# Optimization experiments

Measured on AMD Instinct MI355X. Metric: run time of the kernel, lower is better.

Reference implementation:

```python
import jax, jax.numpy as jnp
import numpy as np

N, E, ESM, H_DIM, HEADS, LAYERS = 20000, 640000, 1280, 256, 8, 3
C = H_DIM // HEADS  # per-head channels = 32
B, M = 4096, 8


def setup_inputs() -> dict:
    key = jax.random.key(0)
    ks = jax.random.split(key, 24)
    s = lambda i, *shp: jax.random.normal(ks[i], shp, dtype=jnp.float32) * 0.02
    inp = {
        'x': jax.random.normal(ks[0], (N, ESM), dtype=jnp.float32),
        'edge_index': jax.random.randint(ks[1], (2, E), 0, N),
        'sites': jax.random.randint(ks[2], (B, M), 0, N),
        'mut_onehot': jax.random.normal(ks[3], (B, M, 20), dtype=jnp.float32),
        'mask': jnp.ones((B, M), dtype=bool),
        # params
        'in_W': s(4, ESM, H_DIM), 'in_b': jnp.zeros((H_DIM,), jnp.float32),
        'gat_W': s(5, LAYERS, H_DIM, HEADS * C),
        'att_src': s(6, LAYERS, HEADS, C), 'att_dst': s(7, LAYERS, HEADS, C),
        'gat_b': jnp.zeros((LAYERS, H_DIM), jnp.float32),
        'ln_g': jnp.ones((LAYERS, H_DIM), jnp.float32),
        'ln_b': jnp.zeros((LAYERS, H_DIM), jnp.float32),
        'me_W1': s(8, 20, H_DIM), 'me_b1': jnp.zeros((H_DIM,), jnp.float32),
        'me_W2': s(9, H_DIM, H_DIM), 'me_b2': jnp.zeros((H_DIM,), jnp.float32),
        'pool_q': jax.random.normal(ks[10], (H_DIM,), dtype=jnp.float32),
        'key_W': s(11, H_DIM, H_DIM), 'key_b': jnp.zeros((H_DIM,), jnp.float32),
        'mlp_W1': s(12, H_DIM, H_DIM // 2), 'mlp_b1': jnp.zeros((H_DIM // 2,), jnp.float32),
        'mlp_W2': s(13, H_DIM // 2, 1), 'mlp_b2': jnp.zeros((1,), jnp.float32),
    }
    return inp


def layer_norm(h, g, b, eps=1e-5):
    mu = h.mean(-1, keepdims=True)
    var = ((h - mu) ** 2).mean(-1, keepdims=True)
    return (h - mu) * jax.lax.rsqrt(var + eps) * g + b


def gat_conv(h, src, dst, W, a_src, a_dst, b):
    # PyG GATConv: linear -> per-node attn logits -> edge leaky_relu -> segment softmax over dst -> scatter-sum
    xh = (h @ W).reshape(N, HEADS, C)
    al_s = (xh * a_src).sum(-1)  # [N,H]
    al_d = (xh * a_dst).sum(-1)
    alpha = jax.nn.leaky_relu(al_s[src] + al_d[dst], negative_slope=0.2)  # [E',H]
    mx = jax.ops.segment_max(alpha, dst, num_segments=N)
    ea = jnp.exp(alpha - mx[dst])
    denom = jax.ops.segment_sum(ea, dst, num_segments=N)
    w = ea / (denom[dst] + 1e-16)
    msg = xh[src] * w[:, :, None]  # [E',H,C]
    out = jax.ops.segment_sum(msg, dst, num_segments=N)
    return out.reshape(N, HEADS * C) + b


def reference(x, edge_index, sites, mut_onehot, mask, in_W, in_b, gat_W, att_src, att_dst,
              gat_b, ln_g, ln_b, me_W1, me_b1, me_W2, me_b2, pool_q, key_W, key_b,
              mlp_W1, mlp_b1, mlp_W2, mlp_b2):
    # GATConv default add_self_loops=True
    loops = jnp.arange(N, dtype=edge_index.dtype)
    src = jnp.concatenate([edge_index[0], loops])
    dst = jnp.concatenate([edge_index[1], loops])
    # encode_graph (eval mode: dropout = identity)
    h = x @ in_W + in_b
    for i in range(LAYERS):
        h_new = gat_conv(h, src, dst, gat_W[i], att_src[i][None], att_dst[i][None], gat_b[i])
        h_new = jax.nn.elu(h_new)
        h = layer_norm(h_new + h, ln_g[i], ln_b[i])
    # predict_batch
    site_embeds = h[sites]  # [B,M,H_DIM]
    mut_embeds = jax.nn.relu(mut_onehot @ me_W1 + me_b1) @ me_W2 + me_b2
    combined = site_embeds + mut_embeds
    keys = combined @ key_W + key_b
    scores = (pool_q * keys).sum(-1) / np.sqrt(H_DIM).astype(np.float32)
    scores = jnp.where(mask, scores, -jnp.inf)
    weights = jax.nn.softmax(scores, axis=-1)[..., None]
    pooled = (weights * combined).sum(axis=1)  # [B,H_DIM]
    out = jax.nn.relu(pooled @ mlp_W1 + mlp_b1) @ mlp_W2 + mlp_b2
    return out.squeeze(-1)
```

## Files before the change

### kernel.cpp

```cpp
#include <hip/hip_runtime.h>
#include <math.h>

#define N_NODES 20000
#define N_EDGES 640000
#define E_TOT   (N_EDGES + N_NODES)
#define HD 256
#define NH 8
#define CH 32
#define NB 4096
#define NM 8

typedef short bf16x8 __attribute__((ext_vector_type(8)));
typedef float f32x4  __attribute__((ext_vector_type(4)));

__device__ __forceinline__ ushort f2bf(float f) {
  uint u = __float_as_uint(f);
  u += 0x7FFFu + ((u >> 16) & 1u);
  return (ushort)(u >> 16);
}
__device__ __forceinline__ float bf2f(ushort s) {
  return __uint_as_float(((uint)s) << 16);
}

__global__ __launch_bounds__(256) void k_wtrans(
    const float* __restrict__ W, ushort* __restrict__ WT,
    int K, int N, int strideW, int strideWT)
{
  __shared__ float tile[64][65];
  const float* Wp = W + (size_t)blockIdx.z * strideW;
  ushort* WTp = WT + (size_t)blockIdx.z * strideWT;
  int n0 = blockIdx.x * 64, k0 = blockIdx.y * 64;
  int t = threadIdx.x;
  int c = t & 63, r0 = (t >> 6) * 16;
#pragma unroll
  for (int i = 0; i < 16; ++i)
    tile[r0 + i][c] = Wp[(size_t)(k0 + r0 + i) * N + n0 + c];
  __syncthreads();
#pragma unroll
  for (int i = 0; i < 16; ++i)
    WTp[(size_t)(n0 + r0 + i) * K + k0 + c] = f2bf(tile[c][r0 + i]);
}

template<int MODE>
__global__ __launch_bounds__(256, 2) void k_gemm_mfma(
    const void* __restrict__ Ain, const ushort* __restrict__ BT,
    const float* __restrict__ bias, float* __restrict__ Cf,
    ushort* __restrict__ Cb, int M, int K)
{
  __shared__ ushort As[128 * 32];
  __shared__ ushort Bs[128 * 32];
  const int t = threadIdx.x;
  const int n0 = blockIdx.x * 128;
  const int m0 = blockIdx.y * 128;
  const int wave = t >> 6, lane = t & 63;
  const int wm = (wave & 1) * 64, wn = (wave >> 1) * 64;
  const int lm = lane & 15, quad = lane >> 4;

  f32x4 acc[4][4];
#pragma unroll
  for (int mi = 0; mi < 4; ++mi)
#pragma unroll
    for (int ni = 0; ni < 4; ++ni) acc[mi][ni] = (f32x4){0.f, 0.f, 0.f, 0.f};

  int rowc[2], jc[2], arc[2];
#pragma unroll
  for (int cch = 0; cch < 2; ++cch) {
    int id = t + cch * 256;
    rowc[cch] = id >> 2;
    jc[cch]   = id & 3;
    arc[cch]  = min(m0 + rowc[cch], M - 1);
  }

  float4 pa0[2], pa1[2];
  uint4  paB[2];
  uint4  pb[2];

#define LOAD_TILE(K0)                                                          \
  {                                                                            \
    _Pragma("unroll")                                                          \
    for (int cch = 0; cch < 2; ++cch) {                                        \
      if (MODE == 0) {                                                         \
        const float* src = (const float*)Ain + (size_t)arc[cch] * K + (K0) + jc[cch] * 8; \
        pa0[cch] = *(const float4*)src;                                        \
        pa1[cch] = *(const float4*)(src + 4);                                  \
      } else {                                                                 \
        const ushort* src = (const ushort*)Ain + (size_t)arc[cch] * K + (K0) + jc[cch] * 8; \
        paB[cch] = *(const uint4*)src;                                         \
      }                                                                        \
      pb[cch] = *(const uint4*)(BT + (size_t)(n0 + rowc[cch]) * K + (K0) + jc[cch] * 8); \
    }                                                                          \
  }

  LOAD_TILE(0);

  for (int k0 = 0; k0 < K; k0 += 32) {
#pragma unroll
    for (int cch = 0; cch < 2; ++cch) {
      int row = rowc[cch];
      int sw = (jc[cch] ^ (row & 3)) * 8;
      if (MODE == 0) {
        uint4 p;
        p.x = (uint)f2bf(pa0[cch].x) | ((uint)f2bf(pa0[cch].y) << 16);
        p.y = (uint)f2bf(pa0[cch].z) | ((uint)f2bf(pa0[cch].w) << 16);
        p.z = (uint)f2bf(pa1[cch].x) | ((uint)f2bf(pa1[cch].y) << 16);
        p.w = (uint)f2bf(pa1[cch].z) | ((uint)f2bf(pa1[cch].w) << 16);
        *(uint4*)&As[row * 32 + sw] = p;
      } else {
        *(uint4*)&As[row * 32 + sw] = paB[cch];
      }
      *(uint4*)&Bs[row * 32 + sw] = pb[cch];
    }
    __syncthreads();
    if (k0 + 32 < K) LOAD_TILE(k0 + 32);

    bf16x8 af[4], bfr[4];
#pragma unroll
    for (int mi = 0; mi < 4; ++mi) {
      int row = wm + mi * 16 + lm;
      af[mi] = *(const bf16x8*)&As[row * 32 + ((quad ^ (row & 3)) << 3)];
    }
#pragma unroll
    for (int ni = 0; ni < 4; ++ni) {
      int row = wn + ni * 16 + lm;
      bfr[ni] = *(const bf16x8*)&Bs[row * 32 + ((quad ^ (row & 3)) << 3)];
    }
#pragma unroll
    for (int mi = 0; mi < 4; ++mi)
#pragma unroll
      for (int ni = 0; ni < 4; ++ni)
        acc[mi][ni] = __builtin_amdgcn_mfma_f32_16x16x32_bf16(af[mi], bfr[ni], acc[mi][ni], 0, 0, 0);
    __syncthreads();
  }
#undef LOAD_TILE

#pragma unroll
  for (int mi = 0; mi < 4; ++mi) {
#pragma unroll
    for (int r = 0; r < 4; ++r) {
      int row = m0 + wm + mi * 16 + quad * 4 + r;
      if (row < M) {
#pragma unroll
        for (int ni = 0; ni < 4; ++ni) {
          int col = n0 + wn + ni * 16 + lm;
          float vv = acc[mi][ni][r];
          if (MODE == 0) {
            float o = vv + bias[col];
            Cf[(size_t)row * HD + col] = o;
            Cb[(size_t)row * HD + col] = f2bf(o);
          } else {
            Cb[(size_t)row * HD + col] = f2bf(vv);
          }
        }
      }
    }
  }
}

__global__ void k_setconst(int* __restrict__ p, int n, int v) {
  int i = blockIdx.x * blockDim.x + threadIdx.x;
  if (i < n) p[i] = v;
}

__global__ void k_count(const int* __restrict__ dst, int* __restrict__ cnt) {
  int e = blockIdx.x * blockDim.x + threadIdx.x;
  if (e < N_EDGES) atomicAdd(&cnt[dst[e]], 1);
}

__global__ __launch_bounds__(1024) void k_scanA(const int* __restrict__ cnt,
                                                int* __restrict__ sc, int* __restrict__ tot) {
  __shared__ int wsum[16];
  int g = blockIdx.x * 1024 + threadIdx.x;
  int lane = threadIdx.x & 63, w = threadIdx.x >> 6;
  int v = (g < N_NODES) ? cnt[g] : 0;
#pragma unroll
  for (int off = 1; off < 64; off <<= 1) {
    int u = __shfl_up(v, off);
    if (lane >= off) v += u;
  }
  if (lane == 63) wsum[w] = v;
  __syncthreads();
  if (w == 0) {
    int s = (lane < 16) ? wsum[lane] : 0;
#pragma unroll
    for (int off = 1; off < 16; off <<= 1) {
      int u = __shfl_up(s, off);
      if (lane >= off) s += u;
    }
    if (lane < 16) wsum[lane] = s;
  }
  __syncthreads();
  if (w > 0) v += wsum[w - 1];
  if (g < N_NODES) sc[g] = v;
  if (threadIdx.x == 1023) tot[blockIdx.x] = v;
}

__global__ void k_scanB(int* __restrict__ tot) {
  int lane = threadIdx.x;
  int v = (lane < 20) ? tot[lane] : 0;
#pragma unroll
  for (int off = 1; off < 32; off <<= 1) {
    int u = __shfl_up(v, off);
    if (lane >= off) v += u;
  }
  int e = __shfl_up(v, 1);
  if (lane == 0) e = 0;
  if (lane < 20) tot[lane] = e;
}

__global__ __launch_bounds__(1024) void k_scanC(const int* __restrict__ sc,
                                                const int* __restrict__ tot,
                                                int* __restrict__ row_ptr) {
  int g = blockIdx.x * 1024 + threadIdx.x;
  if (g < N_NODES) row_ptr[g + 1] = sc[g] + tot[blockIdx.x];
  if (g == 0) row_ptr[0] = 0;
}

__global__ void k_fill(const int* __restrict__ ei, const int* __restrict__ row_ptr,
                       int* __restrict__ fill, int* __restrict__ csr) {
  int idx = blockIdx.x * blockDim.x + threadIdx.x;
  if (idx >= E_TOT) return;
  int s, d;
  if (idx < N_EDGES) { s = ei[idx]; d = ei[N_EDGES + idx]; }
  else               { s = idx - N_EDGES; d = s; }
  int p = atomicAdd(&fill[d], 1);
  csr[row_ptr[d] + p] = s;
}

__global__ void k_attn(const ushort* __restrict__ xh,
                       const float* __restrict__ att_s,
                       const float* __restrict__ att_d,
                       float* __restrict__ al_s, float* __restrict__ al_d)
{
  int idx = blockIdx.x * blockDim.x + threadIdx.x;
  if (idx >= N_NODES * NH) return;
  int hh = idx & 7;
  const ushort* row = xh + (size_t)(idx >> 3) * HD + hh * CH;
  const float4* a4  = (const float4*)(att_s + hh * CH);
  const float4* b4  = (const float4*)(att_d + hh * CH);
  float s = 0.f, d = 0.f;
#pragma unroll
  for (int q = 0; q < 8; ++q) {
    ushort4 xv = *(const ushort4*)(row + q * 4);
    float4 a = a4[q], b = b4[q];
    float v0 = bf2f(xv.x), v1 = bf2f(xv.y), v2 = bf2f(xv.z), v3 = bf2f(xv.w);
    s += v0 * a.x + v1 * a.y + v2 * a.z + v3 * a.w;
    d += v0 * b.x + v1 * b.y + v2 * b.z + v3 * b.w;
  }
  al_s[idx] = s;
  al_d[idx] = d;
}

__global__ __launch_bounds__(256) void k_aggregate(
    const ushort* __restrict__ xh, const float* __restrict__ al_s,
    const float* __restrict__ al_d, const int* __restrict__ row_ptr,
    const int* __restrict__ csr_src, const float* __restrict__ gat_b,
    const float* __restrict__ ln_g, const float* __restrict__ ln_b,
    float* __restrict__ h, ushort* __restrict__ h_bf)
{
  __shared__ float s_ea[4][64][9];
  __shared__ int   s_src[4][64];
  __shared__ int   s_deg[4];
  const int t = threadIdx.x;
  const int w = t >> 6, lane = t & 63;
  const int node = blockIdx.x * 4 + w;
  const int base = row_ptr[node];
  const int deg  = row_ptr[node + 1] - base;
  if (lane == 0) s_deg[w] = deg;
  __syncthreads();
  const int maxdeg = max(max(s_deg[0], s_deg[1]), max(s_deg[2], s_deg[3]));
  const int chunks = (maxdeg + 63) >> 6;

  float ald[8];
  {
    float4 a0 = *(const float4*)(al_d + (size_t)node * NH);
    float4 a1 = *(const float4*)(al_d + (size_t)node * NH + 4);
    ald[0] = a0.x; ald[1] = a0.y; ald[2] = a0.z; ald[3] = a0.w;
    ald[4] = a1.x; ald[5] = a1.y; ald[6] = a1.z; ald[7] = a1.w;
  }
  const int hh = lane >> 3;
  float4 acc = {0.f, 0.f, 0.f, 0.f};
  float den = 0.f;

  for (int c = 0; c < chunks; ++c) {
    const int cs = c << 6;
    int n = deg - cs; n = (n > 64) ? 64 : n;
    if (lane < n) {
      int s = csr_src[base + cs + lane];
      s_src[w][lane] = s;
      float4 b0 = *(const float4*)(al_s + (size_t)s * NH);
      float4 b1 = *(const float4*)(al_s + (size_t)s * NH + 4);
      float al[8] = {b0.x, b0.y, b0.z, b0.w, b1.x, b1.y, b1.z, b1.w};
#pragma unroll
      for (int q = 0; q < 8; ++q) {
        float a = al[q] + ald[q];
        a = fmaxf(a, 0.2f * a);
        s_ea[w][lane][q] = __expf(a);
      }
    }
    __syncthreads();
    for (int e = 0; e < n; ++e) {
      float wa = s_ea[w][e][hh];
      int s = s_src[w][e];
      den += wa;
      ushort4 xv = *(const ushort4*)(xh + (size_t)s * HD + lane * 4);
      acc.x = fmaf(wa, bf2f(xv.x), acc.x);
      acc.y = fmaf(wa, bf2f(xv.y), acc.y);
      acc.z = fmaf(wa, bf2f(xv.z), acc.z);
      acc.w = fmaf(wa, bf2f(xv.w), acc.w);
    }
    __syncthreads();
  }

  const float inv = 1.f / (den + 1e-16f);
  float4 g4 = *(const float4*)(gat_b + lane * 4);
  float4 v;
  v.x = acc.x * inv + g4.x;
  v.y = acc.y * inv + g4.y;
  v.z = acc.z * inv + g4.z;
  v.w = acc.w * inv + g4.w;
  v.x = (v.x > 0.f) ? v.x : (__expf(v.x) - 1.f);
  v.y = (v.y > 0.f) ? v.y : (__expf(v.y) - 1.f);
  v.z = (v.z > 0.f) ? v.z : (__expf(v.z) - 1.f);
  v.w = (v.w > 0.f) ? v.w : (__expf(v.w) - 1.f);
  float4 hres = *(const float4*)(h + (size_t)node * HD + lane * 4);
  v.x += hres.x; v.y += hres.y; v.z += hres.z; v.w += hres.w;

  float sum = v.x + v.y + v.z + v.w;
#pragma unroll
  for (int off = 32; off > 0; off >>= 1) sum += __shfl_xor(sum, off);
  const float mu = sum * (1.f / 256.f);
  float dx = v.x - mu, dy = v.y - mu, dz = v.z - mu, dw = v.w - mu;
  float ss = dx * dx + dy * dy + dz * dz + dw * dw;
#pragma unroll
  for (int off = 32; off > 0; off >>= 1) ss += __shfl_xor(ss, off);
  const float r = rsqrtf(ss * (1.f / 256.f) + 1e-5f);
  float4 lg = *(const float4*)(ln_g + lane * 4);
  float4 lb = *(const float4*)(ln_b + lane * 4);
  float4 o;
  o.x = dx * r * lg.x + lb.x;
  o.y = dy * r * lg.y + lb.y;
  o.z = dz * r * lg.z + lb.z;
  o.w = dw * r * lg.w + lb.w;
  *(float4*)(h + (size_t)node * HD + lane * 4) = o;
  ushort4 ob;
  ob.x = f2bf(o.x); ob.y = f2bf(o.y); ob.z = f2bf(o.z); ob.w = f2bf(o.w);
  *(ushort4*)(h_bf + (size_t)node * HD + lane * 4) = ob;
}

__global__ __launch_bounds__(256) void k_qk(const float* __restrict__ key_W,
                                            const float* __restrict__ key_b,
                                            const float* __restrict__ pool_q,
                                            float* __restrict__ qk)
{
  __shared__ float sq[HD];
  int t = threadIdx.x;
  sq[t] = pool_q[t];
  __syncthreads();
  float a = 0.f;
  for (int j = 0; j < HD; ++j) a = fmaf(key_W[(size_t)t * HD + j], sq[j], a);
  qk[t] = a;
  if (t == 0) {
    float qb = 0.f;
    for (int j = 0; j < HD; ++j) qb += sq[j] * key_b[j];
    qk[HD] = qb;
  }
}

__global__ __launch_bounds__(256) void k_mut1(
    const float* __restrict__ onehot, const float* __restrict__ W1,
    const float* __restrict__ b1, ushort* __restrict__ m1)
{
  __shared__ float s_oh[128][20];
  const int t = threadIdx.x;
  const int r0 = blockIdx.x * 128;
  float wreg[20];
#pragma unroll
  for (int j = 0; j < 20; ++j) wreg[j] = W1[j * HD + t];
  const float bb = b1[t];
  for (int i = t; i < 128 * 20; i += 256)
    s_oh[i / 20][i % 20] = onehot[(size_t)r0 * 20 + i];
  __syncthreads();
  for (int r = 0; r < 128; ++r) {
    float v = bb;
#pragma unroll
    for (int j = 0; j < 20; ++j) v = fmaf(s_oh[r][j], wreg[j], v);
    m1[(size_t)(r0 + r) * HD + t] = f2bf(fmaxf(v, 0.f));
  }
}

__global__ __launch_bounds__(256, 2) void k_gemm_mut2(
    const ushort* __restrict__ m1, const ushort* __restrict__ W2T,
    const float* __restrict__ me_b2, const float* __restrict__ h,
    const int* __restrict__ sites, const unsigned char* __restrict__ mask8,
    const float* __restrict__ qk, float* __restrict__ pooled)
{
  __shared__ ushort As[64 * 32];
  __shared__ ushort Bs[256 * 32];
  __shared__ float s_part[64][4];
  __shared__ float s_w[64];
  __shared__ int   s_site[64];
  const int t = threadIdx.x;
  const int rows0 = blockIdx.x * 64;
  const int wave = t >> 6, lane = t & 63;
  const int wn = wave * 64;
  const int lm = lane & 15, quad = lane >> 4;

  if (t < 64) s_site[t] = sites[rows0 + t];

  f32x4 acc[4][4];
#pragma unroll
  for (int mi = 0; mi < 4; ++mi)
#pragma unroll
    for (int ni = 0; ni < 4; ++ni) acc[mi][ni] = (f32x4){0.f, 0.f, 0.f, 0.f};

  const int a_row = t >> 2, a_j = t & 3;
  uint4 pa;
  uint4 pbv[4];
#define LOAD_MUT(K0)                                                           \
  {                                                                            \
    pa = *(const uint4*)(m1 + (size_t)(rows0 + a_row) * HD + (K0) + a_j * 8);  \
    _Pragma("unroll")                                                          \
    for (int p = 0; p < 4; ++p) {                                              \
      int id = t + p * 256;                                                    \
      int row = id >> 2, j = id & 3;                                           \
      pbv[p] = *(const uint4*)(W2T + (size_t)row * HD + (K0) + j * 8);         \
    }                                                                          \
  }

  LOAD_MUT(0);
  for (int k0 = 0; k0 < HD; k0 += 32) {
    {
      int sw = (a_j ^ (a_row & 3)) * 8;
      *(uint4*)&As[a_row * 32 + sw] = pa;
#pragma unroll
      for (int p = 0; p < 4; ++p) {
        int id = t + p * 256;
        int row = id >> 2, j = id & 3;
        *(uint4*)&Bs[row * 32 + ((j ^ (row & 3)) * 8)] = pbv[p];
      }
    }
    __syncthreads();
    if (k0 + 32 < HD) LOAD_MUT(k0 + 32);

    bf16x8 af[4], bfr[4];
#pragma unroll
    for (int mi = 0; mi < 4; ++mi) {
      int row = mi * 16 + lm;
      af[mi] = *(const bf16x8*)&As[row * 32 + ((quad ^ (row & 3)) << 3)];
    }
#pragma unroll
    for (int ni = 0; ni < 4; ++ni) {
      int row = wn + ni * 16 + lm;
      bfr[ni] = *(const bf16x8*)&Bs[row * 32 + ((quad ^ (row & 3)) << 3)];
    }
#pragma unroll
    for (int mi = 0; mi < 4; ++mi)
#pragma unroll
      for (int ni = 0; ni < 4; ++ni)
        acc[mi][ni] = __builtin_amdgcn_mfma_f32_16x16x32_bf16(af[mi], bfr[ni], acc[mi][ni], 0, 0, 0);
    __syncthreads();
  }
#undef LOAD_MUT

  float pscore[4][4];
#pragma unroll
  for (int mi = 0; mi < 4; ++mi)
#pragma unroll
    for (int r = 0; r < 4; ++r) pscore[mi][r] = 0.f;

#pragma unroll
  for (int ni = 0; ni < 4; ++ni) {
    int col = wn + ni * 16 + lm;
    float qkc = qk[col];
    float b2c = me_b2[col];
#pragma unroll
    for (int mi = 0; mi < 4; ++mi) {
#pragma unroll
      for (int r = 0; r < 4; ++r) {
        int row = mi * 16 + quad * 4 + r;
        float c = acc[mi][ni][r] + b2c + h[(size_t)s_site[row] * HD + col];
        acc[mi][ni][r] = c;
        pscore[mi][r] = fmaf(c, qkc, pscore[mi][r]);
      }
    }
  }
#pragma unroll
  for (int mi = 0; mi < 4; ++mi)
#pragma unroll
    for (int r = 0; r < 4; ++r) {
      float p = pscore[mi][r];
      p += __shfl_xor(p, 8); p += __shfl_xor(p, 4);
      p += __shfl_xor(p, 2); p += __shfl_xor(p, 1);
      pscore[mi][r] = p;
    }
  if (lm == 0) {
#pragma unroll
    for (int mi = 0; mi < 4; ++mi)
#pragma unroll
      for (int r = 0; r < 4; ++r)
        s_part[mi * 16 + quad * 4 + r][wave] = pscore[mi][r];
  }
  __syncthreads();
  if (t < 64) {
    float s = s_part[t][0] + s_part[t][1] + s_part[t][2] + s_part[t][3];
    s = (s + qk[HD]) * 0.0625f;
    int grow = rows0 + t;
    bool mb;
    if (mask8[1] != 0) mb = mask8[grow] != 0;
    else               mb = ((const int*)mask8)[grow] != 0;
    s_w[t] = mb ? s : -INFINITY;
  }
  __syncthreads();
  if (t < 8) {
    float e[NM], mx = -INFINITY, den = 0.f;
#pragma unroll
    for (int m = 0; m < NM; ++m) mx = fmaxf(mx, s_w[t * NM + m]);
#pragma unroll
    for (int m = 0; m < NM; ++m) { e[m] = __expf(s_w[t * NM + m] - mx); den += e[m]; }
    float inv = 1.f / den;
#pragma unroll
    for (int m = 0; m < NM; ++m) s_w[t * NM + m] = e[m] * inv;
  }
  __syncthreads();
#pragma unroll
  for (int ni = 0; ni < 4; ++ni) {
    int col = wn + ni * 16 + lm;
#pragma unroll
    for (int mi = 0; mi < 4; ++mi) {
      float pp = 0.f;
#pragma unroll
      for (int r = 0; r < 4; ++r)
        pp = fmaf(s_w[mi * 16 + quad * 4 + r], acc[mi][ni][r], pp);
      pp += __shfl_xor(pp, 16);
      int b = mi * 2 + (quad >> 1);
      if ((quad & 1) == 0)
        pooled[(size_t)(blockIdx.x * 8 + b) * HD + col] = pp;
    }
  }
}

__global__ __launch_bounds__(128) void k_mlp(
    const float* __restrict__ pooled, const float* __restrict__ W1,
    const float* __restrict__ b1, const float* __restrict__ W2,
    const float* __restrict__ b2, float* __restrict__ out)
{
  __shared__ float s_p[16][256];
  __shared__ float s_red[16][128];
  const int t = threadIdx.x;
  const int r0 = blockIdx.x * 16;
  for (int i = t; i < 16 * 256; i += 128) {
    int r = i >> 8, cc = i & 255;
    s_p[r][cc] = pooled[(size_t)(r0 + r) * HD + cc];
  }
  __syncthreads();
  float accm[16];
#pragma unroll
  for (int r = 0; r < 16; ++r) accm[r] = 0.f;
  for (int i = 0; i < 256; ++i) {
    float w = W1[(size_t)i * 128 + t];
#pragma unroll
    for (int r = 0; r < 16; ++r) accm[r] = fmaf(s_p[r][i], w, accm[r]);
  }
  float w2 = W2[t], bb1 = b1[t];
#pragma unroll
  for (int r = 0; r < 16; ++r) s_red[r][t] = fmaxf(accm[r] + bb1, 0.f) * w2;
  __syncthreads();
  if (t < 16) {
    float s = b2[0];
    for (int j = 0; j < 128; ++j) s += s_red[t][j];
    out[r0 + t] = s;
  }
}

extern "C" void kernel_launch(void* const* d_in, const int* in_sizes, int n_in,
                              void* d_out, int out_size, void* d_ws, size_t ws_size,
                              hipStream_t stream) {
  (void)in_sizes; (void)n_in; (void)out_size; (void)ws_size;
  const float* x        = (const float*)d_in[0];
  const int*   ei       = (const int*)d_in[1];
  const int*   sites    = (const int*)d_in[2];
  const float* onehot   = (const float*)d_in[3];
  const unsigned char* mask = (const unsigned char*)d_in[4];
  const float* in_W     = (const float*)d_in[5];
  const float* in_b     = (const float*)d_in[6];
  const float* gat_W    = (const float*)d_in[7];
  const float* att_src  = (const float*)d_in[8];
  const float* att_dst  = (const float*)d_in[9];
  const float* gat_b    = (const float*)d_in[10];
  const float* ln_g     = (const float*)d_in[11];
  const float* ln_b     = (const float*)d_in[12];
  const float* me_W1    = (const float*)d_in[13];
  const float* me_b1    = (const float*)d_in[14];
  const float* me_W2    = (const float*)d_in[15];
  const float* me_b2    = (const float*)d_in[16];
  const float* pool_q   = (const float*)d_in[17];
  const float* key_W    = (const float*)d_in[18];
  const float* key_b    = (const float*)d_in[19];
  const float* mlp_W1   = (const float*)d_in[20];
  const float* mlp_b1   = (const float*)d_in[21];
  const float* mlp_W2   = (const float*)d_in[22];
  const float* mlp_b2   = (const float*)d_in[23];
  float* outp = (float*)d_out;

  char* w = (char*)d_ws;
  float*  h       = (float*)(w + 0);
  ushort* h_bf    = (ushort*)(w + 20480000);
  ushort* xh_bf   = (ushort*)(w + 30720000);
  float*  al_s    = (float*)(w + 40960000);
  float*  al_d    = (float*)(w + 41600000);
  int*    row_ptr = (int*)  (w + 42240000);
  int*    cnt     = (int*)  (w + 42320128);
  int*    csr     = (int*)  (w + 42400128);
  float*  qk      = (float*)(w + 45040128);
  float*  pooled  = (float*)(w + 45041408);
  int*    sc      = (int*)pooled;
  int*    tot     = sc + N_NODES;
  ushort* in_WT   = (ushort*)((char*)pooled + 131072);
  ushort* gat_WT  = (ushort*)((char*)pooled + 786432);
  ushort* m1      = (ushort*)(w + 20480000);
  ushort* me_W2T  = (ushort*)(w + 40960000);

  k_wtrans<<<dim3(4, 20, 1), 256, 0, stream>>>(in_W, in_WT, 1280, HD, 0, 0);
  k_wtrans<<<dim3(4, 4, 3), 256, 0, stream>>>(gat_W, gat_WT, HD, HD, HD * HD, HD * HD);

  k_gemm_mfma<0><<<dim3(2, 157), 256, 0, stream>>>(x, in_WT, in_b, h, h_bf, N_NODES, 1280);

  k_setconst<<<(N_NODES + 255) / 256, 256, 0, stream>>>(cnt, N_NODES, 1);
  k_count<<<(N_EDGES + 255) / 256, 256, 0, stream>>>(ei + N_EDGES, cnt);
  k_scanA<<<20, 1024, 0, stream>>>(cnt, sc, tot);
  k_scanB<<<1, 64, 0, stream>>>(tot);
  k_scanC<<<20, 1024, 0, stream>>>(sc, tot, row_ptr);
  k_setconst<<<(N_NODES + 255) / 256, 256, 0, stream>>>(cnt, N_NODES, 0);
  k_fill<<<(E_TOT + 255) / 256, 256, 0, stream>>>(ei, row_ptr, cnt, csr);

  for (int l = 0; l < 3; ++l) {
    k_gemm_mfma<1><<<dim3(2, 157), 256, 0, stream>>>(h_bf, gat_WT + (size_t)l * HD * HD,
                                                     nullptr, nullptr, xh_bf, N_NODES, HD);
    k_attn<<<(N_NODES * NH + 255) / 256, 256, 0, stream>>>(xh_bf, att_src + l * NH * CH,
                                                           att_dst + l * NH * CH, al_s, al_d);
    k_aggregate<<<N_NODES / 4, 256, 0, stream>>>(xh_bf, al_s, al_d, row_ptr, csr,
                                                 gat_b + l * HD, ln_g + l * HD, ln_b + l * HD,
                                                 h, h_bf);
  }

  k_wtrans<<<dim3(4, 4, 1), 256, 0, stream>>>(me_W2, me_W2T, HD, HD, 0, 0);
  k_mut1<<<NB * NM / 128, 256, 0, stream>>>(onehot, me_W1, me_b1, m1);
  k_qk<<<1, 256, 0, stream>>>(key_W, key_b, pool_q, qk);
  k_gemm_mut2<<<NB * NM / 64, 256, 0, stream>>>(m1, me_W2T, me_b2, h, sites, mask, qk, pooled);
  k_mlp<<<NB / 16, 128, 0, stream>>>(pooled, mlp_W1, mlp_b1, mlp_W2, mlp_b2, outp);
}
```

Before: 699.7 us.

## Shrink GEMM M-tile to 64, drop register prefetch, split aggregate edges across half-waves

The node GEMM's M-tile drops from 128 to 64 rows, with launch bounds raised to 4 blocks per CU and the grid doubled, for more occupancy and better load balance. The register prefetch of the next K tile is removed from both GEMMs, simplifying them at the cost of less overlap between loads and MFMA. The aggregation kernel now has each half-wave handle alternate edges with 16-byte loads of 8 channels, combining the halves with a shuffle. This doubles memory-level parallelism per gather but adds a reduction and leaves half the lanes idle during the stores.

```diff
diff --git a/kernel.cpp b/kernel.cpp
--- a/kernel.cpp
+++ b/kernel.cpp
@@ -42,80 +42,56 @@
 }
 
 template<int MODE>
-__global__ __launch_bounds__(256, 2) void k_gemm_mfma(
+__global__ __launch_bounds__(256, 4) void k_gemm_mfma(
     const void* __restrict__ Ain, const ushort* __restrict__ BT,
     const float* __restrict__ bias, float* __restrict__ Cf,
     ushort* __restrict__ Cb, int M, int K)
 {
-  __shared__ ushort As[128 * 32];
+  __shared__ ushort As[64 * 32];
   __shared__ ushort Bs[128 * 32];
   const int t = threadIdx.x;
   const int n0 = blockIdx.x * 128;
-  const int m0 = blockIdx.y * 128;
+  const int m0 = blockIdx.y * 64;
   const int wave = t >> 6, lane = t & 63;
-  const int wm = (wave & 1) * 64, wn = (wave >> 1) * 64;
+  const int wm = (wave & 1) * 32, wn = (wave >> 1) * 64;
   const int lm = lane & 15, quad = lane >> 4;
 
-  f32x4 acc[4][4];
-#pragma unroll
-  for (int mi = 0; mi < 4; ++mi)
+  f32x4 acc[2][4];
+#pragma unroll
+  for (int mi = 0; mi < 2; ++mi)
 #pragma unroll
     for (int ni = 0; ni < 4; ++ni) acc[mi][ni] = (f32x4){0.f, 0.f, 0.f, 0.f};
 
-  int rowc[2], jc[2], arc[2];
-#pragma unroll
-  for (int cch = 0; cch < 2; ++cch) {
-    int id = t + cch * 256;
-    rowc[cch] = id >> 2;
-    jc[cch]   = id & 3;
-    arc[cch]  = min(m0 + rowc[cch], M - 1);
-  }
-
-  float4 pa0[2], pa1[2];
-  uint4  paB[2];
-  uint4  pb[2];
-
-#define LOAD_TILE(K0)                                                          \
-  {                                                                            \
-    _Pragma("unroll")                                                          \
-    for (int cch = 0; cch < 2; ++cch) {                                        \
-      if (MODE == 0) {                                                         \
-        const float* src = (const float*)Ain + (size_t)arc[cch] * K + (K0) + jc[cch] * 8; \
-        pa0[cch] = *(const float4*)src;                                        \
-        pa1[cch] = *(const float4*)(src + 4);                                  \
-      } else {                                                                 \
-        const ushort* src = (const ushort*)Ain + (size_t)arc[cch] * K + (K0) + jc[cch] * 8; \
-        paB[cch] = *(const uint4*)src;                                         \
-      }                                                                        \
-      pb[cch] = *(const uint4*)(BT + (size_t)(n0 + rowc[cch]) * K + (K0) + jc[cch] * 8); \
-    }                                                                          \
-  }
-
-  LOAD_TILE(0);
+  const int a_row = t >> 2, a_j = t & 3;
+  const int ar = min(m0 + a_row, M - 1);
+  const int a_sw = (a_j ^ (a_row & 3)) * 8;
 
   for (int k0 = 0; k0 < K; k0 += 32) {
-#pragma unroll
-    for (int cch = 0; cch < 2; ++cch) {
-      int row = rowc[cch];
-      int sw = (jc[cch] ^ (row & 3)) * 8;
-      if (MODE == 0) {
-        uint4 p;
-        p.x = (uint)f2bf(pa0[cch].x) | ((uint)f2bf(pa0[cch].y) << 16);
-        p.y = (uint)f2bf(pa0[cch].z) | ((uint)f2bf(pa0[cch].w) << 16);
-        p.z = (uint)f2bf(pa1[cch].x) | ((uint)f2bf(pa1[cch].y) << 16);
-        p.w = (uint)f2bf(pa1[cch].z) | ((uint)f2bf(pa1[cch].w) << 16);
-        *(uint4*)&As[row * 32 + sw] = p;
-      } else {
-        *(uint4*)&As[row * 32 + sw] = paB[cch];
-      }
-      *(uint4*)&Bs[row * 32 + sw] = pb[cch];
+    if (MODE == 0) {
+      const float* src = (const float*)Ain + (size_t)ar * K + k0 + a_j * 8;
+      float4 u = *(const float4*)src;
+      float4 v = *(const float4*)(src + 4);
+      uint4 p;
+      p.x = (uint)f2bf(u.x) | ((uint)f2bf(u.y) << 16);
+      p.y = (uint)f2bf(u.z) | ((uint)f2bf(u.w) << 16);
+      p.z = (uint)f2bf(v.x) | ((uint)f2bf(v.y) << 16);
+      p.w = (uint)f2bf(v.z) | ((uint)f2bf(v.w) << 16);
+      *(uint4*)&As[a_row * 32 + a_sw] = p;
+    } else {
+      const ushort* src = (const ushort*)Ain + (size_t)ar * K + k0 + a_j * 8;
+      *(uint4*)&As[a_row * 32 + a_sw] = *(const uint4*)src;
+    }
+#pragma unroll
+    for (int p = 0; p < 2; ++p) {
+      int id = t + p * 256;
+      int row = id >> 2, j = id & 3;
+      *(uint4*)&Bs[row * 32 + ((j ^ (row & 3)) * 8)] =
+          *(const uint4*)(BT + (size_t)(n0 + row) * K + k0 + j * 8);
     }
     __syncthreads();
-    if (k0 + 32 < K) LOAD_TILE(k0 + 32);
-
-    bf16x8 af[4], bfr[4];
-#pragma unroll
-    for (int mi = 0; mi < 4; ++mi) {
+    bf16x8 af[2], bfr[4];
+#pragma unroll
+    for (int mi = 0; mi < 2; ++mi) {
       int row = wm + mi * 16 + lm;
       af[mi] = *(const bf16x8*)&As[row * 32 + ((quad ^ (row & 3)) << 3)];
     }
@@ -125,16 +101,15 @@
       bfr[ni] = *(const bf16x8*)&Bs[row * 32 + ((quad ^ (row & 3)) << 3)];
     }
 #pragma unroll
-    for (int mi = 0; mi < 4; ++mi)
+    for (int mi = 0; mi < 2; ++mi)
 #pragma unroll
       for (int ni = 0; ni < 4; ++ni)
         acc[mi][ni] = __builtin_amdgcn_mfma_f32_16x16x32_bf16(af[mi], bfr[ni], acc[mi][ni], 0, 0, 0);
     __syncthreads();
   }
-#undef LOAD_TILE
-
-#pragma unroll
-  for (int mi = 0; mi < 4; ++mi) {
+
+#pragma unroll
+  for (int mi = 0; mi < 2; ++mi) {
 #pragma unroll
     for (int r = 0; r < 4; ++r) {
       int row = m0 + wm + mi * 16 + quad * 4 + r;
@@ -262,6 +237,7 @@
   __shared__ int   s_deg[4];
   const int t = threadIdx.x;
   const int w = t >> 6, lane = t & 63;
+  const int lane32 = lane & 31, hw = lane >> 5;
   const int node = blockIdx.x * 4 + w;
   const int base = row_ptr[node];
   const int deg  = row_ptr[node + 1] - base;
@@ -277,8 +253,8 @@
     ald[0] = a0.x; ald[1] = a0.y; ald[2] = a0.z; ald[3] = a0.w;
     ald[4] = a1.x; ald[5] = a1.y; ald[6] = a1.z; ald[7] = a1.w;
   }
-  const int hh = lane >> 3;
-  float4 acc = {0.f, 0.f, 0.f, 0.f};
+  const int myhead = lane32 >> 2;
+  float acc[8] = {0.f, 0.f, 0.f, 0.f, 0.f, 0.f, 0.f, 0.f};
   float den = 0.f;
 
   for (int c = 0; c < chunks; ++c) {
@@ -298,53 +274,84 @@
       }
     }
     __syncthreads();
-    for (int e = 0; e < n; ++e) {
-      float wa = s_ea[w][e][hh];
-      int s = s_src[w][e];
-      den += wa;
-      ushort4 xv = *(const ushort4*)(xh + (size_t)s * HD + lane * 4);
-      acc.x = fmaf(wa, bf2f(xv.x), acc.x);
-      acc.y = fmaf(wa, bf2f(xv.y), acc.y);
-      acc.z = fmaf(wa, bf2f(xv.z), acc.z);
-      acc.w = fmaf(wa, bf2f(xv.w), acc.w);
+    for (int e = 0; e < n; e += 2) {
+      int my_e = e + hw;
+      if (my_e < n) {
+        int s = s_src[w][my_e];
+        float wa = s_ea[w][my_e][myhead];
+        den += wa;
+        uint4 xv = *(const uint4*)(xh + (size_t)s * HD + lane32 * 8);
+        ushort e0 = (ushort)(xv.x & 0xFFFF), e1 = (ushort)(xv.x >> 16);
+        ushort e2 = (ushort)(xv.y & 0xFFFF), e3 = (ushort)(xv.y >> 16);
+        ushort e4 = (ushort)(xv.z & 0xFFFF), e5 = (ushort)(xv.z >> 16);
+        ushort e6 = (ushort)(xv.w & 0xFFFF), e7 = (ushort)(xv.w >> 16);
+        acc[0] = fmaf(wa, bf2f(e0), acc[0]);
+        acc[1] = fmaf(wa, bf2f(e1), acc[1]);
+        acc[2] = fmaf(wa, bf2f(e2), acc[2]);
+        acc[3] = fmaf(wa, bf2f(e3), acc[3]);
+        acc[4] = fmaf(wa, bf2f(e4), acc[4]);
+        acc[5] = fmaf(wa, bf2f(e5), acc[5]);
+        acc[6] = fmaf(wa, bf2f(e6), acc[6]);
+        acc[7] = fmaf(wa, bf2f(e7), acc[7]);
+      }
     }
     __syncthreads();
   }
 
+#pragma unroll
+  for (int q = 0; q < 8; ++q) acc[q] += __shfl_xor(acc[q], 32);
+  den += __shfl_xor(den, 32);
+
   const float inv = 1.f / (den + 1e-16f);
-  float4 g4 = *(const float4*)(gat_b + lane * 4);
-  float4 v;
-  v.x = acc.x * inv + g4.x;
-  v.y = acc.y * inv + g4.y;
-  v.z = acc.z * inv + g4.z;
-  v.w = acc.w * inv + g4.w;
-  v.x = (v.x > 0.f) ? v.x : (__expf(v.x) - 1.f);
-  v.y = (v.y > 0.f) ? v.y : (__expf(v.y) - 1.f);
-  v.z = (v.z > 0.f) ? v.z : (__expf(v.z) - 1.f);
-  v.w = (v.w > 0.f) ? v.w : (__expf(v.w) - 1.f);
-  float4 hres = *(const float4*)(h + (size_t)node * HD + lane * 4);
-  v.x += hres.x; v.y += hres.y; v.z += hres.z; v.w += hres.w;
-
-  float sum = v.x + v.y + v.z + v.w;
-#pragma unroll
-  for (int off = 32; off > 0; off >>= 1) sum += __shfl_xor(sum, off);
-  const float mu = sum * (1.f / 256.f);
-  float dx = v.x - mu, dy = v.y - mu, dz = v.z - mu, dw = v.w - mu;
-  float ss = dx * dx + dy * dy + dz * dz + dw * dw;
-#pragma unroll
-  for (int off = 32; off > 0; off >>= 1) ss += __shfl_xor(ss, off);
-  const float r = rsqrtf(ss * (1.f / 256.f) + 1e-5f);
-  float4 lg = *(const float4*)(ln_g + lane * 4);
-  float4 lb = *(const float4*)(ln_b + lane * 4);
-  float4 o;
-  o.x = dx * r * lg.x + lb.x;
-  o.y = dy * r * lg.y + lb.y;
-  o.z = dz * r * lg.z + lb.z;
-  o.w = dw * r * lg.w + lb.w;
-  *(float4*)(h + (size_t)node * HD + lane * 4) = o;
-  ushort4 ob;
-  ob.x = f2bf(o.x); ob.y = f2bf(o.y); ob.z = f2bf(o.z); ob.w = f2bf(o.w);
-  *(ushort4*)(h_bf + (size_t)node * HD + lane * 4) = ob;
+  const int c8 = lane32 * 8;
+  float4 g0 = *(const float4*)(gat_b + c8);
+  float4 g1 = *(const float4*)(gat_b + c8 + 4);
+  float gb[8] = {g0.x, g0.y, g0.z, g0.w, g1.x, g1.y, g1.z, g1.w};
+  float4 h0 = *(const float4*)(h + (size_t)node * HD + c8);
+  float4 h1 = *(const float4*)(h + (size_t)node * HD + c8 + 4);
+  float hr[8] = {h0.x, h0.y, h0.z, h0.w, h1.x, h1.y, h1.z, h1.w};
+  float v[8], sum8 = 0.f;
+#pragma unroll
+  for (int q = 0; q < 8; ++q) {
+    float vv = acc[q] * inv + gb[q];
+    vv = (vv > 0.f) ? vv : (__expf(vv) - 1.f);
+    vv += hr[q];
+    v[q] = vv;
+    sum8 += vv;
+  }
+#pragma unroll
+  for (int off = 32; off > 0; off >>= 1) sum8 += __shfl_xor(sum8, off);
+  const float mu = sum8 * (1.f / 512.f);
+  float ss8 = 0.f;
+#pragma unroll
+  for (int q = 0; q < 8; ++q) {
+    v[q] -= mu;
+    ss8 = fmaf(v[q], v[q], ss8);
+  }
+#pragma unroll
+  for (int off = 32; off > 0; off >>= 1) ss8 += __shfl_xor(ss8, off);
+  const float r = rsqrtf(ss8 * (1.f / 512.f) + 1e-5f);
+  if (hw == 0) {
+    float4 lg0 = *(const float4*)(ln_g + c8);
+    float4 lg1 = *(const float4*)(ln_g + c8 + 4);
+    float4 lb0 = *(const float4*)(ln_b + c8);
+    float4 lb1 = *(const float4*)(ln_b + c8 + 4);
+    float lg[8] = {lg0.x, lg0.y, lg0.z, lg0.w, lg1.x, lg1.y, lg1.z, lg1.w};
+    float lb[8] = {lb0.x, lb0.y, lb0.z, lb0.w, lb1.x, lb1.y, lb1.z, lb1.w};
+    float o[8];
+#pragma unroll
+    for (int q = 0; q < 8; ++q) o[q] = v[q] * r * lg[q] + lb[q];
+    float4 of0 = {o[0], o[1], o[2], o[3]};
+    float4 of1 = {o[4], o[5], o[6], o[7]};
+    *(float4*)(h + (size_t)node * HD + c8) = of0;
+    *(float4*)(h + (size_t)node * HD + c8 + 4) = of1;
+    uint4 ob;
+    ob.x = (uint)f2bf(o[0]) | ((uint)f2bf(o[1]) << 16);
+    ob.y = (uint)f2bf(o[2]) | ((uint)f2bf(o[3]) << 16);
+    ob.z = (uint)f2bf(o[4]) | ((uint)f2bf(o[5]) << 16);
+    ob.w = (uint)f2bf(o[6]) | ((uint)f2bf(o[7]) << 16);
+    *(uint4*)(h_bf + (size_t)node * HD + c8) = ob;
+  }
 }
 
 __global__ __launch_bounds__(256) void k_qk(const float* __restrict__ key_W,
@@ -414,34 +421,17 @@
     for (int ni = 0; ni < 4; ++ni) acc[mi][ni] = (f32x4){0.f, 0.f, 0.f, 0.f};
 
   const int a_row = t >> 2, a_j = t & 3;
-  uint4 pa;
-  uint4 pbv[4];
-#define LOAD_MUT(K0)                                                           \
-  {                                                                            \
-    pa = *(const uint4*)(m1 + (size_t)(rows0 + a_row) * HD + (K0) + a_j * 8);  \
-    _Pragma("unroll")                                                          \
-    for (int p = 0; p < 4; ++p) {                                              \
-      int id = t + p * 256;                                                    \
-      int row = id >> 2, j = id & 3;                                           \
-      pbv[p] = *(const uint4*)(W2T + (size_t)row * HD + (K0) + j * 8);         \
-    }                                                                          \
-  }
-
-  LOAD_MUT(0);
   for (int k0 = 0; k0 < HD; k0 += 32) {
-    {
-      int sw = (a_j ^ (a_row & 3)) * 8;
-      *(uint4*)&As[a_row * 32 + sw] = pa;
-#pragma unroll
-      for (int p = 0; p < 4; ++p) {
-        int id = t + p * 256;
-        int row = id >> 2, j = id & 3;
-        *(uint4*)&Bs[row * 32 + ((j ^ (row & 3)) * 8)] = pbv[p];
-      }
+    *(uint4*)&As[a_row * 32 + ((a_j ^ (a_row & 3)) * 8)] =
+        *(const uint4*)(m1 + (size_t)(rows0 + a_row) * HD + k0 + a_j * 8);
+#pragma unroll
+    for (int p = 0; p < 4; ++p) {
+      int id = t + p * 256;
+      int row = id >> 2, j = id & 3;
+      *(uint4*)&Bs[row * 32 + ((j ^ (row & 3)) * 8)] =
+          *(const uint4*)(W2T + (size_t)row * HD + k0 + j * 8);
     }
     __syncthreads();
-    if (k0 + 32 < HD) LOAD_MUT(k0 + 32);
-
     bf16x8 af[4], bfr[4];
 #pragma unroll
     for (int mi = 0; mi < 4; ++mi) {
@@ -460,7 +450,6 @@
         acc[mi][ni] = __builtin_amdgcn_mfma_f32_16x16x32_bf16(af[mi], bfr[ni], acc[mi][ni], 0, 0, 0);
     __syncthreads();
   }
-#undef LOAD_MUT
 
   float pscore[4][4];
 #pragma unroll
@@ -623,7 +612,7 @@
   k_wtrans<<<dim3(4, 20, 1), 256, 0, stream>>>(in_W, in_WT, 1280, HD, 0, 0);
   k_wtrans<<<dim3(4, 4, 3), 256, 0, stream>>>(gat_W, gat_WT, HD, HD, HD * HD, HD * HD);
 
-  k_gemm_mfma<0><<<dim3(2, 157), 256, 0, stream>>>(x, in_WT, in_b, h, h_bf, N_NODES, 1280);
+  k_gemm_mfma<0><<<dim3(2, 313), 256, 0, stream>>>(x, in_WT, in_b, h, h_bf, N_NODES, 1280);
 
   k_setconst<<<(N_NODES + 255) / 256, 256, 0, stream>>>(cnt, N_NODES, 1);
   k_count<<<(N_EDGES + 255) / 256, 256, 0, stream>>>(ei + N_EDGES, cnt);
@@ -634,7 +623,7 @@
   k_fill<<<(E_TOT + 255) / 256, 256, 0, stream>>>(ei, row_ptr, cnt, csr);
 
   for (int l = 0; l < 3; ++l) {
-    k_gemm_mfma<1><<<dim3(2, 157), 256, 0, stream>>>(h_bf, gat_WT + (size_t)l * HD * HD,
+    k_gemm_mfma<1><<<dim3(2, 313), 256, 0, stream>>>(h_bf, gat_WT + (size_t)l * HD * HD,
                                                      nullptr, nullptr, xh_bf, N_NODES, HD);
     k_attn<<<(N_NODES * NH + 255) / 256, 256, 0, stream>>>(xh_bf, att_src + l * NH * CH,
                                                            att_dst + l * NH * CH, al_s, al_d);
```

Measured after the change: 621.7 us. -11.1%, faster.
